# Kernel tuning notes

Measured on AMD Instinct MI355X. Metric: run time of the kernel, lower is better.

The kernel has to match this reference:

```python
import jax, jax.numpy as jnp
import numpy as np

T, H, I, E, K = 1024, 1024, 1024, 16, 8
INIT_STD = 0.02


def setup_inputs() -> dict:
    key = jax.random.key(0)
    k0, k1, k2, k3, k4 = jax.random.split(key, 5)
    hidden_states = jax.random.normal(k0, (T, H), dtype=jnp.float32)
    top_k_index = jax.random.randint(k1, (T, K), 0, E, dtype=jnp.int64)
    top_k_weights = jax.random.uniform(k2, (T, K), dtype=jnp.float32)
    gate_up_proj = jax.random.normal(k3, (E, 2 * I, H), dtype=jnp.float32) * INIT_STD
    down_proj = jax.random.normal(k4, (E, H, I), dtype=jnp.float32) * INIT_STD
    return {
        "hidden_states": hidden_states,
        "top_k_index": top_k_index,
        "top_k_weights": top_k_weights,
        "gate_up_proj": gate_up_proj,
        "down_proj": down_proj,
    }


def reference(hidden_states, top_k_index, top_k_weights, gate_up_proj, down_proj):
    # hidden_states: [T, H]; gate_up_proj: [E, 2I, H]; down_proj: [E, H, I]
    num_tokens = hidden_states.shape[0]
    num_experts = gate_up_proj.shape[0]

    # Per-token combine weights: scatter top_k_weights into a dense [T, E] map.
    # Tokens not routed to expert e get weight 0, so the dense all-expert
    # compute below is mathematically identical to the masked gather/scatter loop.
    token_ids = jnp.arange(num_tokens)[:, None]  # [T, 1]
    combine = jnp.zeros((num_tokens, num_experts), dtype=hidden_states.dtype)
    combine = combine.at[token_ids, top_k_index].add(top_k_weights)  # [T, E]

    # Gated MLP for every (token, expert) pair.
    gate_up = jnp.einsum("th,eoh->teo", hidden_states, gate_up_proj)  # [T, E, 2I]
    gate, up = jnp.split(gate_up, 2, axis=-1)
    act = jax.nn.silu(gate) * up  # [T, E, I]
    down = jnp.einsum("tei,ehi->teh", act, down_proj)  # [T, E, H]

    # Weighted combine over experts (zero weight -> no contribution).
    return jnp.einsum("teh,te->th", down, combine)  # [T, H]
```

## Files before the change

### kernel.cpp

```cpp
#include <hip/hip_runtime.h>
#include <cstdint>
#include <cstddef>

#define TT 1024
#define HH 1024
#define IW 1024
#define EE 16
#define KK 8
#define NSLOT (TT*KK)

typedef unsigned short u16;
typedef unsigned int   u32;
typedef __attribute__((ext_vector_type(4))) float f32x4;
typedef __attribute__((ext_vector_type(8))) short s16x8;
typedef __attribute__((ext_vector_type(8))) u16   u16x8;

__device__ __forceinline__ u16 f2bf(float f) {
  union { float f; u32 u; } v; v.f = f;
  u32 u = v.u + 0x7fffu + ((v.u >> 16) & 1u);
  return (u16)(u >> 16);
}

__device__ __forceinline__ void gload16(const void* g, void* l) {
  __builtin_amdgcn_global_load_lds(
      (const __attribute__((address_space(1))) u32*)g,
      (__attribute__((address_space(3))) u32*)l, 16, 0, 0);
}

#define MFMA16(a, b, c) __builtin_amdgcn_mfma_f32_16x16x32_bf16((a), (b), (c), 0, 0, 0)


__global__ void k_cvtx(const float* __restrict__ hs, u16* __restrict__ xb) {
  int g = blockIdx.x * 256 + threadIdx.x;
  const f32x4* s = (const f32x4*)(hs + (size_t)g * 8);
  f32x4 f0 = s[0], f1 = s[1];
  u16x8 p;
#pragma unroll
  for (int i = 0; i < 4; ++i) { p[i] = f2bf(f0[i]); p[i + 4] = f2bf(f1[i]); }
  *(u16x8*)(xb + (size_t)g * 8) = p;
}

__global__ void k_count(const int* __restrict__ idx, int* __restrict__ counts) {
  for (int s = blockIdx.x * 256 + threadIdx.x; s < NSLOT; s += gridDim.x * 256)
    atomicAdd(&counts[idx[s]], 1);
}

__global__ void k_scan(const int* __restrict__ counts, int* __restrict__ offsets,
                       int* __restrict__ cursor) {
  if (threadIdx.x == 0) {
    int r = 0;
    for (int e = 0; e < EE; ++e) { offsets[e] = r; cursor[e] = r; r += counts[e]; }
    offsets[EE] = r;
  }
}

__global__ void k_scatter(const int* __restrict__ idx, int* __restrict__ cursor,
                          int* __restrict__ slot_token, int* __restrict__ inv) {
  for (int s = blockIdx.x * 256 + threadIdx.x; s < NSLOT; s += gridDim.x * 256) {
    int e = idx[s];
    int pos = atomicAdd(&cursor[e], 1);
    slot_token[pos] = s >> 3;
    inv[s] = pos;
  }
}


__global__ __launch_bounds__(256, 2) void k_gemm1(
    const u16* __restrict__ xb,
    const float* __restrict__ gup,
    const int* __restrict__ offsets,
    const int* __restrict__ slot_token,
    u16* __restrict__ act)
{
  __shared__ __align__(16) u16 As[128 * 32];
  __shared__ __align__(16) u16 Bgs[64 * 32];
  __shared__ __align__(16) u16 Bus[64 * 32];

  const int e = blockIdx.z, mt = blockIdx.y, nt = blockIdx.x;
  const int off = offsets[e];
  const int ne  = offsets[e + 1] - off;
  if (mt * 128 >= ne) return;

  const int tid = threadIdx.x;
  const int lane = tid & 63, wid = tid >> 6;
  const int wm = wid >> 1, wn = wid & 1;

  const int l4 = lane >> 2;
  const int lq = lane & 3;
  const int chunk = lq ^ (l4 & 3);
  int tok[2];
#pragma unroll
  for (int q = 0; q < 2; ++q) {
    int grow = mt * 128 + q * 64 + wid * 16 + l4;
    if (grow >= ne) grow = ne - 1;
    tok[q] = slot_token[off + grow];
  }

  const int bwhich = tid >> 7;
  const int bidx = tid & 127;
  const int br = bidx >> 1, bh = bidx & 1;
  const size_t browg = (size_t)(bwhich ? (IW + nt * 64 + br) : (nt * 64 + br));
  const float* bsrc0 = gup + ((size_t)e * 2 * IW + browg) * HH;
  u16* Bt = bwhich ? Bus : Bgs;
  const int bq0 = (((2 * bh + 0) ^ (br & 3)) << 3);
  const int bq1 = (((2 * bh + 1) ^ (br & 3)) << 3);

  f32x4 accg[4][2], accu[4][2];
  const f32x4 zz = {0.f, 0.f, 0.f, 0.f};
#pragma unroll
  for (int m = 0; m < 4; ++m)
#pragma unroll
    for (int n = 0; n < 2; ++n) { accg[m][n] = zz; accu[m][n] = zz; }

  const int r16 = lane & 15, kg = lane >> 4;
  const int rq = ((kg ^ (r16 & 3)) << 3);

  for (int kk = 0; kk < HH / 32; ++kk) {
    const int k0 = kk * 32;
#pragma unroll
    for (int q = 0; q < 2; ++q)
      gload16(xb + (size_t)tok[q] * HH + k0 + chunk * 8,
              As + (q * 64 + wid * 16) * 32);
    {
      const f32x4* s = (const f32x4*)(bsrc0 + k0 + bh * 16);
      f32x4 f0 = s[0], f1 = s[1], f2 = s[2], f3 = s[3];
      u16x8 p0, p1;
#pragma unroll
      for (int i = 0; i < 4; ++i) {
        p0[i] = f2bf(f0[i]); p0[i + 4] = f2bf(f1[i]);
        p1[i] = f2bf(f2[i]); p1[i + 4] = f2bf(f3[i]);
      }
      *(u16x8*)(Bt + br * 32 + bq0) = p0;
      *(u16x8*)(Bt + br * 32 + bq1) = p1;
    }
    __syncthreads();

    s16x8 a[4], bg[2], bu[2];
#pragma unroll
    for (int m = 0; m < 4; ++m)
      a[m] = *(const s16x8*)(As + (wm * 64 + m * 16 + r16) * 32 + rq);
#pragma unroll
    for (int n = 0; n < 2; ++n) {
      bg[n] = *(const s16x8*)(Bgs + (wn * 32 + n * 16 + r16) * 32 + rq);
      bu[n] = *(const s16x8*)(Bus + (wn * 32 + n * 16 + r16) * 32 + rq);
    }
#pragma unroll
    for (int m = 0; m < 4; ++m)
#pragma unroll
      for (int n = 0; n < 2; ++n) {
        accg[m][n] = MFMA16(a[m], bg[n], accg[m][n]);
        accu[m][n] = MFMA16(a[m], bu[n], accu[m][n]);
      }
    __syncthreads();
  }

#pragma unroll
  for (int m = 0; m < 4; ++m) {
    const int baserow = mt * 128 + wm * 64 + m * 16 + kg * 4;
#pragma unroll
    for (int n = 0; n < 2; ++n) {
      const int c = nt * 64 + wn * 32 + n * 16 + r16;
#pragma unroll
      for (int j = 0; j < 4; ++j) {
        const int row = baserow + j;
        if (row < ne) {
          float g = accg[m][n][j], u = accu[m][n][j];
          float sv = g / (1.f + __expf(-g));
          act[(size_t)(off + row) * IW + c] = f2bf(sv * u);
        }
      }
    }
  }
}


__global__ __launch_bounds__(256, 2) void k_gemm2(
    const u16* __restrict__ act,
    const float* __restrict__ dp,
    const int* __restrict__ offsets,
    float* __restrict__ wdown)
{
  __shared__ __align__(16) u16 As[128 * 32];
  __shared__ __align__(16) u16 Bs[128 * 32];

  const int e = blockIdx.z, mt = blockIdx.y, nt = blockIdx.x;
  const int off = offsets[e];
  const int ne  = offsets[e + 1] - off;
  if (mt * 128 >= ne) return;

  const int tid = threadIdx.x;
  const int lane = tid & 63, wid = tid >> 6;
  const int wm = wid >> 1, wn = wid & 1;

  const int l4 = lane >> 2, lq = lane & 3;
  const int chunk = lq ^ (l4 & 3);
  int arow[2];
#pragma unroll
  for (int q = 0; q < 2; ++q) {
    int grow = mt * 128 + q * 64 + wid * 16 + l4;
    if (grow >= ne) grow = ne - 1;
    arow[q] = off + grow;
  }

  const int br = tid >> 1, bh = tid & 1;
  const float* bsrc0 = dp + ((size_t)e * HH + nt * 128 + br) * IW;
  const int bq0 = (((2 * bh + 0) ^ (br & 3)) << 3);
  const int bq1 = (((2 * bh + 1) ^ (br & 3)) << 3);

  f32x4 acc[4][4];
  const f32x4 zz = {0.f, 0.f, 0.f, 0.f};
#pragma unroll
  for (int m = 0; m < 4; ++m)
#pragma unroll
    for (int n = 0; n < 4; ++n) acc[m][n] = zz;

  const int r16 = lane & 15, kg = lane >> 4;
  const int rq = ((kg ^ (r16 & 3)) << 3);

  for (int kk = 0; kk < IW / 32; ++kk) {
    const int k0 = kk * 32;
#pragma unroll
    for (int q = 0; q < 2; ++q)
      gload16(act + (size_t)arow[q] * IW + k0 + chunk * 8,
              As + (q * 64 + wid * 16) * 32);
    {
      const f32x4* s = (const f32x4*)(bsrc0 + k0 + bh * 16);
      f32x4 f0 = s[0], f1 = s[1], f2 = s[2], f3 = s[3];
      u16x8 p0, p1;
#pragma unroll
      for (int i = 0; i < 4; ++i) {
        p0[i] = f2bf(f0[i]); p0[i + 4] = f2bf(f1[i]);
        p1[i] = f2bf(f2[i]); p1[i + 4] = f2bf(f3[i]);
      }
      *(u16x8*)(Bs + br * 32 + bq0) = p0;
      *(u16x8*)(Bs + br * 32 + bq1) = p1;
    }
    __syncthreads();

    s16x8 a[4], b[4];
#pragma unroll
    for (int m = 0; m < 4; ++m)
      a[m] = *(const s16x8*)(As + (wm * 64 + m * 16 + r16) * 32 + rq);
#pragma unroll
    for (int n = 0; n < 4; ++n)
      b[n] = *(const s16x8*)(Bs + (wn * 64 + n * 16 + r16) * 32 + rq);
#pragma unroll
    for (int m = 0; m < 4; ++m)
#pragma unroll
      for (int n = 0; n < 4; ++n)
        acc[m][n] = MFMA16(a[m], b[n], acc[m][n]);
    __syncthreads();
  }

#pragma unroll
  for (int m = 0; m < 4; ++m) {
    const int baserow = mt * 128 + wm * 64 + m * 16 + kg * 4;
#pragma unroll
    for (int n = 0; n < 4; ++n) {
      const int h = nt * 128 + wn * 64 + n * 16 + r16;
#pragma unroll
      for (int j = 0; j < 4; ++j) {
        const int row = baserow + j;
        if (row < ne)
          wdown[(size_t)(off + row) * HH + h] = acc[m][n][j];
      }
    }
  }
}


__global__ void k_combine(const float* __restrict__ wdown, const int* __restrict__ inv,
                          const float* __restrict__ tkw, float* __restrict__ out) {
  int g = blockIdx.x * 256 + threadIdx.x;
  int t = g >> 8;
  int hv = (g & 255) * 4;
  f32x4 a = {0.f, 0.f, 0.f, 0.f};
#pragma unroll
  for (int k = 0; k < KK; ++k) {
    int pos = inv[t * KK + k];
    float w = tkw[t * KK + k];
    f32x4 v = *(const f32x4*)(wdown + (size_t)pos * HH + hv);
    a += w * v;
  }
  *(f32x4*)(out + (size_t)t * HH + hv) = a;
}


extern "C" void kernel_launch(void* const* d_in, const int* in_sizes, int n_in,
                              void* d_out, int out_size, void* d_ws, size_t ws_size,
                              hipStream_t stream) {
  const float* hs  = (const float*)d_in[0];
  const int*   idx = (const int*)d_in[1];
  const float* tkw = (const float*)d_in[2];
  const float* gup = (const float*)d_in[3];
  const float* dpw = (const float*)d_in[4];
  float* out = (float*)d_out;

  char* ws = (char*)d_ws;
  size_t o = 0;
  u16* xb = (u16*)(ws + o);         o += (size_t)TT * HH * 2;
  int* counts  = (int*)(ws + o);    o += 64;
  int* cursor  = (int*)(ws + o);    o += 64;
  int* offsets = (int*)(ws + o);    o += 128;
  int* slot_token = (int*)(ws + o); o += (size_t)NSLOT * 4;
  int* inv     = (int*)(ws + o);    o += (size_t)NSLOT * 4;
  o = (o + 255) & ~(size_t)255;
  u16* act = (u16*)(ws + o);        o += (size_t)NSLOT * IW * 2;
  float* wdown = (float*)(ws + o);  o += (size_t)NSLOT * HH * 4;

  hipMemsetAsync(counts, 0, 64, stream);
  k_cvtx<<<TT * HH / (256 * 8), 256, 0, stream>>>(hs, xb);
  k_count<<<16, 256, 0, stream>>>(idx, counts);
  k_scan<<<1, 64, 0, stream>>>(counts, offsets, cursor);
  k_scatter<<<16, 256, 0, stream>>>(idx, cursor, slot_token, inv);
  k_gemm1<<<dim3(IW / 64, NSLOT / 128, EE), 256, 0, stream>>>(xb, gup, offsets, slot_token, act);
  k_gemm2<<<dim3(HH / 128, NSLOT / 128, EE), 256, 0, stream>>>(act, dpw, offsets, wdown);
  k_combine<<<TT * HH / 4 / 256, 256, 0, stream>>>(wdown, inv, tkw, out);
}
```

Before: 431.2 us.

## Pre-convert expert weights to bf16 and use compact tile list with LDS-direct loads

Adds conversion kernels that turn the fp32 gate_up and down projection weights into bf16 once per call, so both GEMMs stream bf16 weights into shared memory with global_load_lds instead of converting fp32 in registers per tile. The grid is replaced by a compacted list of (expert, m-tile) pairs built in the scan kernel, avoiding launching empty blocks. The routing weight is folded into the gemm1 epilogue so the combine just sums rows, and the LDS swizzle pattern is changed. The trade-off is an extra full pass over the weights for conversion and a larger workspace.

```diff
diff --git a/kernel.cpp b/kernel.cpp
--- a/kernel.cpp
+++ b/kernel.cpp
@@ -8,6 +8,7 @@
 #define EE 16
 #define KK 8
 #define NSLOT (TT*KK)
+#define NTMAX 80
 
 typedef unsigned short u16;
 typedef unsigned int   u32;
@@ -30,14 +31,14 @@
 #define MFMA16(a, b, c) __builtin_amdgcn_mfma_f32_16x16x32_bf16((a), (b), (c), 0, 0, 0)
 
 
-__global__ void k_cvtx(const float* __restrict__ hs, u16* __restrict__ xb) {
+__global__ void k_cvt(const float* __restrict__ src, u16* __restrict__ dst) {
   int g = blockIdx.x * 256 + threadIdx.x;
-  const f32x4* s = (const f32x4*)(hs + (size_t)g * 8);
+  const f32x4* s = (const f32x4*)(src + (size_t)g * 8);
   f32x4 f0 = s[0], f1 = s[1];
   u16x8 p;
 #pragma unroll
   for (int i = 0; i < 4; ++i) { p[i] = f2bf(f0[i]); p[i + 4] = f2bf(f1[i]); }
-  *(u16x8*)(xb + (size_t)g * 8) = p;
+  *(u16x8*)(dst + (size_t)g * 8) = p;
 }
 
 __global__ void k_count(const int* __restrict__ idx, int* __restrict__ counts) {
@@ -46,20 +47,29 @@
 }
 
 __global__ void k_scan(const int* __restrict__ counts, int* __restrict__ offsets,
-                       int* __restrict__ cursor) {
+                       int* __restrict__ cursor, int* __restrict__ tile_e,
+                       int* __restrict__ tile_mt) {
   if (threadIdx.x == 0) {
-    int r = 0;
-    for (int e = 0; e < EE; ++e) { offsets[e] = r; cursor[e] = r; r += counts[e]; }
+    int r = 0, t = 0;
+    for (int e = 0; e < EE; ++e) {
+      offsets[e] = r; cursor[e] = r;
+      int c = counts[e];
+      for (int mt = 0; mt * 128 < c; ++mt) { tile_e[t] = e; tile_mt[t] = mt; ++t; }
+      r += c;
+    }
     offsets[EE] = r;
-  }
-}
-
-__global__ void k_scatter(const int* __restrict__ idx, int* __restrict__ cursor,
-                          int* __restrict__ slot_token, int* __restrict__ inv) {
+    for (; t < NTMAX; ++t) tile_e[t] = -1;
+  }
+}
+
+__global__ void k_scatter(const int* __restrict__ idx, const float* __restrict__ tkw,
+                          int* __restrict__ cursor, int* __restrict__ slot_token,
+                          float* __restrict__ slot_w, int* __restrict__ inv) {
   for (int s = blockIdx.x * 256 + threadIdx.x; s < NSLOT; s += gridDim.x * 256) {
     int e = idx[s];
     int pos = atomicAdd(&cursor[e], 1);
     slot_token[pos] = s >> 3;
+    slot_w[pos] = tkw[s];
     inv[s] = pos;
   }
 }
@@ -67,19 +77,23 @@
 
 __global__ __launch_bounds__(256, 2) void k_gemm1(
     const u16* __restrict__ xb,
-    const float* __restrict__ gup,
+    const u16* __restrict__ gupb,
     const int* __restrict__ offsets,
     const int* __restrict__ slot_token,
+    const float* __restrict__ slot_w,
+    const int* __restrict__ tile_e,
+    const int* __restrict__ tile_mt,
     u16* __restrict__ act)
 {
   __shared__ __align__(16) u16 As[128 * 32];
   __shared__ __align__(16) u16 Bgs[64 * 32];
   __shared__ __align__(16) u16 Bus[64 * 32];
 
-  const int e = blockIdx.z, mt = blockIdx.y, nt = blockIdx.x;
+  const int e = tile_e[blockIdx.y];
+  if (e < 0) return;
+  const int mt = tile_mt[blockIdx.y], nt = blockIdx.x;
   const int off = offsets[e];
   const int ne  = offsets[e + 1] - off;
-  if (mt * 128 >= ne) return;
 
   const int tid = threadIdx.x;
   const int lane = tid & 63, wid = tid >> 6;
@@ -87,23 +101,22 @@
 
   const int l4 = lane >> 2;
   const int lq = lane & 3;
-  const int chunk = lq ^ (l4 & 3);
-  int tok[2];
+  const int chunk = lq ^ ((l4 >> 1) & 3);
+
+  const u16* asrc[2];
 #pragma unroll
   for (int q = 0; q < 2; ++q) {
     int grow = mt * 128 + q * 64 + wid * 16 + l4;
     if (grow >= ne) grow = ne - 1;
-    tok[q] = slot_token[off + grow];
-  }
-
-  const int bwhich = tid >> 7;
-  const int bidx = tid & 127;
-  const int br = bidx >> 1, bh = bidx & 1;
-  const size_t browg = (size_t)(bwhich ? (IW + nt * 64 + br) : (nt * 64 + br));
-  const float* bsrc0 = gup + ((size_t)e * 2 * IW + browg) * HH;
-  u16* Bt = bwhich ? Bus : Bgs;
-  const int bq0 = (((2 * bh + 0) ^ (br & 3)) << 3);
-  const int bq1 = (((2 * bh + 1) ^ (br & 3)) << 3);
+    asrc[q] = xb + (size_t)slot_token[off + grow] * HH + chunk * 8;
+  }
+  const int bch = nt * 64 + wid * 16 + l4;
+  const u16* bgsrc = gupb + ((size_t)e * 2 * IW + bch) * HH + chunk * 8;
+  const u16* busrc = bgsrc + (size_t)IW * HH;
+  u16* const adst0 = As + (0 * 64 + wid * 16) * 32;
+  u16* const adst1 = As + (1 * 64 + wid * 16) * 32;
+  u16* const bgdst = Bgs + (wid * 16) * 32;
+  u16* const budst = Bus + (wid * 16) * 32;
 
   f32x4 accg[4][2], accu[4][2];
   const f32x4 zz = {0.f, 0.f, 0.f, 0.f};
@@ -113,26 +126,14 @@
     for (int n = 0; n < 2; ++n) { accg[m][n] = zz; accu[m][n] = zz; }
 
   const int r16 = lane & 15, kg = lane >> 4;
-  const int rq = ((kg ^ (r16 & 3)) << 3);
+  const int rq = ((kg ^ ((r16 >> 1) & 3)) << 3);
 
   for (int kk = 0; kk < HH / 32; ++kk) {
     const int k0 = kk * 32;
-#pragma unroll
-    for (int q = 0; q < 2; ++q)
-      gload16(xb + (size_t)tok[q] * HH + k0 + chunk * 8,
-              As + (q * 64 + wid * 16) * 32);
-    {
-      const f32x4* s = (const f32x4*)(bsrc0 + k0 + bh * 16);
-      f32x4 f0 = s[0], f1 = s[1], f2 = s[2], f3 = s[3];
-      u16x8 p0, p1;
-#pragma unroll
-      for (int i = 0; i < 4; ++i) {
-        p0[i] = f2bf(f0[i]); p0[i + 4] = f2bf(f1[i]);
-        p1[i] = f2bf(f2[i]); p1[i + 4] = f2bf(f3[i]);
-      }
-      *(u16x8*)(Bt + br * 32 + bq0) = p0;
-      *(u16x8*)(Bt + br * 32 + bq1) = p1;
-    }
+    gload16(asrc[0] + k0, adst0);
+    gload16(asrc[1] + k0, adst1);
+    gload16(bgsrc + k0, bgdst);
+    gload16(busrc + k0, budst);
     __syncthreads();
 
     s16x8 a[4], bg[2], bu[2];
@@ -166,7 +167,7 @@
         if (row < ne) {
           float g = accg[m][n][j], u = accu[m][n][j];
           float sv = g / (1.f + __expf(-g));
-          act[(size_t)(off + row) * IW + c] = f2bf(sv * u);
+          act[(size_t)(off + row) * IW + c] = f2bf(sv * u * slot_w[off + row]);
         }
       }
     }
@@ -176,36 +177,44 @@
 
 __global__ __launch_bounds__(256, 2) void k_gemm2(
     const u16* __restrict__ act,
-    const float* __restrict__ dp,
+    const u16* __restrict__ dpb,
     const int* __restrict__ offsets,
+    const int* __restrict__ tile_e,
+    const int* __restrict__ tile_mt,
     float* __restrict__ wdown)
 {
   __shared__ __align__(16) u16 As[128 * 32];
   __shared__ __align__(16) u16 Bs[128 * 32];
 
-  const int e = blockIdx.z, mt = blockIdx.y, nt = blockIdx.x;
+  const int e = tile_e[blockIdx.y];
+  if (e < 0) return;
+  const int mt = tile_mt[blockIdx.y], nt = blockIdx.x;
   const int off = offsets[e];
   const int ne  = offsets[e + 1] - off;
-  if (mt * 128 >= ne) return;
 
   const int tid = threadIdx.x;
   const int lane = tid & 63, wid = tid >> 6;
   const int wm = wid >> 1, wn = wid & 1;
 
   const int l4 = lane >> 2, lq = lane & 3;
-  const int chunk = lq ^ (l4 & 3);
-  int arow[2];
+  const int chunk = lq ^ ((l4 >> 1) & 3);
+
+  const u16* asrc[2];
 #pragma unroll
   for (int q = 0; q < 2; ++q) {
     int grow = mt * 128 + q * 64 + wid * 16 + l4;
     if (grow >= ne) grow = ne - 1;
-    arow[q] = off + grow;
-  }
-
-  const int br = tid >> 1, bh = tid & 1;
-  const float* bsrc0 = dp + ((size_t)e * HH + nt * 128 + br) * IW;
-  const int bq0 = (((2 * bh + 0) ^ (br & 3)) << 3);
-  const int bq1 = (((2 * bh + 1) ^ (br & 3)) << 3);
+    asrc[q] = act + (size_t)(off + grow) * IW + chunk * 8;
+  }
+  const u16* bsrc[2];
+#pragma unroll
+  for (int q = 0; q < 2; ++q)
+    bsrc[q] = dpb + ((size_t)e * HH + nt * 128 + q * 64 + wid * 16 + l4) * IW + chunk * 8;
+
+  u16* const adst0 = As + (0 * 64 + wid * 16) * 32;
+  u16* const adst1 = As + (1 * 64 + wid * 16) * 32;
+  u16* const bdst0 = Bs + (0 * 64 + wid * 16) * 32;
+  u16* const bdst1 = Bs + (1 * 64 + wid * 16) * 32;
 
   f32x4 acc[4][4];
   const f32x4 zz = {0.f, 0.f, 0.f, 0.f};
@@ -215,26 +224,14 @@
     for (int n = 0; n < 4; ++n) acc[m][n] = zz;
 
   const int r16 = lane & 15, kg = lane >> 4;
-  const int rq = ((kg ^ (r16 & 3)) << 3);
+  const int rq = ((kg ^ ((r16 >> 1) & 3)) << 3);
 
   for (int kk = 0; kk < IW / 32; ++kk) {
     const int k0 = kk * 32;
-#pragma unroll
-    for (int q = 0; q < 2; ++q)
-      gload16(act + (size_t)arow[q] * IW + k0 + chunk * 8,
-              As + (q * 64 + wid * 16) * 32);
-    {
-      const f32x4* s = (const f32x4*)(bsrc0 + k0 + bh * 16);
-      f32x4 f0 = s[0], f1 = s[1], f2 = s[2], f3 = s[3];
-      u16x8 p0, p1;
-#pragma unroll
-      for (int i = 0; i < 4; ++i) {
-        p0[i] = f2bf(f0[i]); p0[i + 4] = f2bf(f1[i]);
-        p1[i] = f2bf(f2[i]); p1[i + 4] = f2bf(f3[i]);
-      }
-      *(u16x8*)(Bs + br * 32 + bq0) = p0;
-      *(u16x8*)(Bs + br * 32 + bq1) = p1;
-    }
+    gload16(asrc[0] + k0, adst0);
+    gload16(asrc[1] + k0, adst1);
+    gload16(bsrc[0] + k0, bdst0);
+    gload16(bsrc[1] + k0, bdst1);
     __syncthreads();
 
     s16x8 a[4], b[4];
@@ -270,7 +267,7 @@
 
 
 __global__ void k_combine(const float* __restrict__ wdown, const int* __restrict__ inv,
-                          const float* __restrict__ tkw, float* __restrict__ out) {
+                          float* __restrict__ out) {
   int g = blockIdx.x * 256 + threadIdx.x;
   int t = g >> 8;
   int hv = (g & 255) * 4;
@@ -278,9 +275,8 @@
 #pragma unroll
   for (int k = 0; k < KK; ++k) {
     int pos = inv[t * KK + k];
-    float w = tkw[t * KK + k];
     f32x4 v = *(const f32x4*)(wdown + (size_t)pos * HH + hv);
-    a += w * v;
+    a += v;
   }
   *(f32x4*)(out + (size_t)t * HH + hv) = a;
 }
@@ -298,22 +294,30 @@
 
   char* ws = (char*)d_ws;
   size_t o = 0;
-  u16* xb = (u16*)(ws + o);         o += (size_t)TT * HH * 2;
+  u16* xb   = (u16*)(ws + o);       o += (size_t)TT * HH * 2;
+  u16* gupb = (u16*)(ws + o);       o += (size_t)EE * 2 * IW * HH * 2;
+  u16* dpb  = (u16*)(ws + o);       o += (size_t)EE * HH * IW * 2;
   int* counts  = (int*)(ws + o);    o += 64;
   int* cursor  = (int*)(ws + o);    o += 64;
   int* offsets = (int*)(ws + o);    o += 128;
+  int* tile_e  = (int*)(ws + o);    o += NTMAX * 4;
+  int* tile_mt = (int*)(ws + o);    o += NTMAX * 4;
   int* slot_token = (int*)(ws + o); o += (size_t)NSLOT * 4;
   int* inv     = (int*)(ws + o);    o += (size_t)NSLOT * 4;
+  float* slot_w = (float*)(ws + o); o += (size_t)NSLOT * 4;
   o = (o + 255) & ~(size_t)255;
   u16* act = (u16*)(ws + o);        o += (size_t)NSLOT * IW * 2;
   float* wdown = (float*)(ws + o);  o += (size_t)NSLOT * HH * 4;
 
   hipMemsetAsync(counts, 0, 64, stream);
-  k_cvtx<<<TT * HH / (256 * 8), 256, 0, stream>>>(hs, xb);
+  k_cvt<<<TT * HH / (256 * 8), 256, 0, stream>>>(hs, xb);
+  k_cvt<<<(int)((size_t)EE * 2 * IW * HH / (256 * 8)), 256, 0, stream>>>(gup, gupb);
+  k_cvt<<<(int)((size_t)EE * HH * IW / (256 * 8)), 256, 0, stream>>>(dpw, dpb);
   k_count<<<16, 256, 0, stream>>>(idx, counts);
-  k_scan<<<1, 64, 0, stream>>>(counts, offsets, cursor);
-  k_scatter<<<16, 256, 0, stream>>>(idx, cursor, slot_token, inv);
-  k_gemm1<<<dim3(IW / 64, NSLOT / 128, EE), 256, 0, stream>>>(xb, gup, offsets, slot_token, act);
-  k_gemm2<<<dim3(HH / 128, NSLOT / 128, EE), 256, 0, stream>>>(act, dpw, offsets, wdown);
-  k_combine<<<TT * HH / 4 / 256, 256, 0, stream>>>(wdown, inv, tkw, out);
-}
+  k_scan<<<1, 64, 0, stream>>>(counts, offsets, cursor, tile_e, tile_mt);
+  k_scatter<<<16, 256, 0, stream>>>(idx, tkw, cursor, slot_token, slot_w, inv);
+  k_gemm1<<<dim3(IW / 64, NTMAX), 256, 0, stream>>>(xb, gupb, offsets, slot_token,
+                                                    slot_w, tile_e, tile_mt, act);
+  k_gemm2<<<dim3(HH / 128, NTMAX), 256, 0, stream>>>(act, dpb, offsets, tile_e, tile_mt, wdown);
+  k_combine<<<TT * HH / 4 / 256, 256, 0, stream>>>(wdown, inv, out);
+}
```

Result: faster. 410.5 us (-4.8%).
